# Optimization experiments

Hardware: AMD Instinct MI355X
Metric: run time of the kernel (lower is better)

Reference implementation:

```python
import jax, jax.numpy as jnp
import numpy as np

B, N, DIM = 2, 4096, 512
HEADS, HEAD_DIM = 8, 64
INNER = HEADS * HEAD_DIM


def setup_inputs() -> dict:
    key = jax.random.key(0)
    k1, k2, k3 = jax.random.split(key, 3)
    x = jax.random.normal(k1, (B, N, DIM), dtype=jnp.float32)
    w_qkv = jax.random.normal(k2, (DIM, 3 * INNER), dtype=jnp.float32) * (DIM ** -0.5)
    temperature = jnp.asarray(np.log(HEAD_DIM ** -0.5), dtype=jnp.float32)
    w_out = jax.random.normal(k3, (INNER, DIM), dtype=jnp.float32) * (INNER ** -0.5)
    b_out = jnp.zeros((DIM,), dtype=jnp.float32)
    return {"x": x, "w_qkv": w_qkv, "temperature": temperature, "w_out": w_out, "b_out": b_out}


def reference(x, w_qkv, temperature, w_out, b_out):
    b, n, _ = x.shape
    qkv = x @ w_qkv                                   # (B, N, 3*inner)
    q, k, v = jnp.split(qkv, 3, axis=-1)
    # Faithful to original: raw reshape (NOT transpose) into (B, H, N, d)
    q = q.reshape(b, HEADS, n, HEAD_DIM)
    k = k.reshape(b, HEADS, n, HEAD_DIM)
    v = v.reshape(b, HEADS, n, HEAD_DIM)
    scores = jnp.einsum('bhnd,bhmd->bhnm', q, k) * jnp.exp(temperature)
    mask = jnp.eye(n, dtype=bool)                     # diagonal self-mask
    mask_value = jnp.finfo(scores.dtype).min
    scores = jnp.where(mask, mask_value, scores)
    attn = jax.nn.softmax(scores, axis=-1)
    out = jnp.einsum('bhnm,bhmd->bhnd', attn, v)      # (B, H, N, d)
    # Faithful to original: raw reshape (NOT transpose) back to (B, N, H*d)
    out = out.reshape(b, n, HEADS * HEAD_DIM)
    return out @ w_out + b_out                        # dropout inactive at inference
```

## Files before the change

### kernel.cpp

```cpp
#include <hip/hip_runtime.h>


typedef __bf16 bf16;
typedef __bf16 bf16x8 __attribute__((ext_vector_type(8)));
typedef __bf16 bf16x4 __attribute__((ext_vector_type(4)));
typedef __bf16 bf16x2 __attribute__((ext_vector_type(2)));
typedef float  f32x4  __attribute__((ext_vector_type(4)));
typedef float  f32x16 __attribute__((ext_vector_type(16)));
typedef unsigned u32x4 __attribute__((ext_vector_type(4)));

#define MFMA_BF16(a, b, c)   __builtin_amdgcn_mfma_f32_16x16x32_bf16((a), (b), (c), 0, 0, 0)
#define MFMA32_BF16(a, b, c) __builtin_amdgcn_mfma_f32_32x32x16_bf16((a), (b), (c), 0, 0, 0)

__device__ __forceinline__ void gld_lds16(void* lds, const void* g) {
  __builtin_amdgcn_global_load_lds(
      (const __attribute__((address_space(1))) void*)g,
      (__attribute__((address_space(3))) void*)lds, 16, 0, 0);
}

__device__ __forceinline__ unsigned pkbf(float a, float b) {
  bf16x2 t; t[0] = (bf16)a; t[1] = (bf16)b;
  return __builtin_bit_cast(unsigned, t);
}


__global__ void cast4_kernel(const float* __restrict__ in, bf16* __restrict__ out, int n4) {
  int i = blockIdx.x * 256 + threadIdx.x;
  if (i >= n4) return;
  float4 v = ((const float4*)in)[i];
  bf16x4 o;
  o[0] = (bf16)v.x; o[1] = (bf16)v.y; o[2] = (bf16)v.z; o[3] = (bf16)v.w;
  *(bf16x4*)(out + 4 * i) = o;
}

__global__ void wtrans_kernel(const float* __restrict__ in, bf16* __restrict__ out, int C) {
  __shared__ float tile[64 * 65];
  const int t = threadIdx.x;
  const int c0 = blockIdx.x * 64, r0 = blockIdx.y * 64;
#pragma unroll
  for (int p = 0; p < 16; p++) {
    int idx = p * 256 + t, r = idx >> 6, c = idx & 63;
    tile[r * 65 + c] = in[(r0 + r) * C + c0 + c];
  }
  __syncthreads();
#pragma unroll
  for (int p = 0; p < 16; p++) {
    int idx = p * 256 + t, c = idx >> 6, r = idx & 63;
    out[(size_t)(c0 + c) * 512 + r0 + r] = (bf16)tile[r * 65 + c];
  }
}

__global__ void vtrans_kernel(const bf16* __restrict__ V, bf16* __restrict__ Vt) {
  __shared__ bf16 tile[64 * 65];
  const int t = threadIdx.x;
  const size_t base = (size_t)blockIdx.y << 18;
  const int n0 = blockIdx.x * 64;
#pragma unroll
  for (int p = 0; p < 16; p++) {
    int idx = p * 256 + t, r = idx >> 6, c = idx & 63;
    tile[r * 65 + c] = V[base + (size_t)(n0 + r) * 64 + c];
  }
  __syncthreads();
#pragma unroll
  for (int p = 0; p < 16; p++) {
    int idx = p * 256 + t, d = idx >> 6, n = idx & 63;
    Vt[base + (size_t)d * 4096 + n0 + n] = tile[n * 65 + d];
  }
}


template<int EPI, int WNT>
__global__ __launch_bounds__(256) void gemm_bt(
    const bf16* __restrict__ A, const bf16* __restrict__ Bt,
    bf16* __restrict__ oQ, bf16* __restrict__ oK, bf16* __restrict__ oV,
    float* __restrict__ oC, const float* __restrict__ bias,
    const float* __restrict__ temp)
{
  __shared__ bf16 As[128 * 32];
  __shared__ bf16 Bs[WNT * 32 * 32];

  const int t    = threadIdx.x;
  const int lane = t & 63;
  const int w    = t >> 6;
  const int mm   = lane & 15;
  const int q    = lane >> 4;
  const int wm   = w >> 1, wn = w & 1;
  const int m0   = blockIdx.y * 128;
  const int n0   = blockIdx.x * (WNT * 32);

  const int srow = t >> 2, sch = t & 3;
  const int gch  = sch ^ ((srow >> 1) & 3);
  const bf16* Ab = A  + (m0 + srow) * 512 + gch * 8;
  const bf16* Bb = Bt + (n0 + srow) * 512 + gch * 8;
  bf16* Asl = As + t * 8;
  bf16* Bsl = Bs + t * 8;

  const int fslot = (q ^ ((mm >> 1) & 3)) * 8;

  const f32x4 zero4 = {0.f, 0.f, 0.f, 0.f};
  f32x4 acc[4][WNT];
#pragma unroll
  for (int i = 0; i < 4; i++)
#pragma unroll
    for (int j = 0; j < WNT; j++) acc[i][j] = zero4;

  for (int k0 = 0; k0 < 512; k0 += 32) {
    __syncthreads();
    gld_lds16(Asl,        Ab + k0);
    gld_lds16(Asl + 2048, Ab + 64 * 512 + k0);
    gld_lds16(Bsl,        Bb + k0);
    if (WNT == 4) gld_lds16(Bsl + 2048, Bb + 64 * 512 + k0);
    __syncthreads();

    bf16x8 af[4], bfv[WNT];
#pragma unroll
    for (int i = 0; i < 4; i++)
      af[i] = *(const bf16x8*)(As + (wm * 64 + i * 16 + mm) * 32 + fslot);
#pragma unroll
    for (int j = 0; j < WNT; j++)
      bfv[j] = *(const bf16x8*)(Bs + (wn * (WNT * 16) + j * 16 + mm) * 32 + fslot);

#pragma unroll
    for (int i = 0; i < 4; i++)
#pragma unroll
      for (int j = 0; j < WNT; j++)
        acc[i][j] = MFMA_BF16(af[i], bfv[j], acc[i][j]);
  }

  if (EPI == 0) {
    const float scale = __expf(temp[0]) * 1.44269504088896f;
#pragma unroll
    for (int i = 0; i < 4; i++) {
      const int row = m0 + wm * 64 + i * 16 + q * 4;
#pragma unroll
      for (int j = 0; j < WNT; j++) {
        const int col = n0 + wn * (WNT * 16) + j * 16 + mm;
        bf16* dst; int c2; float s;
        if (col < 512)       { dst = oQ; c2 = col;        s = scale; }
        else if (col < 1024) { dst = oK; c2 = col - 512;  s = 1.0f;  }
        else                 { dst = oV; c2 = col - 1024; s = 1.0f;  }
#pragma unroll
        for (int r = 0; r < 4; r++)
          dst[(size_t)(row + r) * 512 + c2] = (bf16)(acc[i][j][r] * s);
      }
    }
  } else {
#pragma unroll
    for (int i = 0; i < 4; i++) {
      const int row = m0 + wm * 64 + i * 16 + q * 4;
#pragma unroll
      for (int j = 0; j < WNT; j++) {
        const int col = n0 + wn * (WNT * 16) + j * 16 + mm;
        const float b = bias[col];
#pragma unroll
        for (int r = 0; r < 4; r++)
          oC[(size_t)(row + r) * 512 + col] = acc[i][j][r] + b;
      }
    }
  }
}


__global__ __launch_bounds__(256, 2) void attn_kernel(
    const bf16* __restrict__ Q, const bf16* __restrict__ Kb,
    const bf16* __restrict__ Vt, bf16* __restrict__ O)
{
  __shared__ bf16 Ks[2][64 * 64];
  __shared__ bf16 Vs[2][64 * 64];
  __shared__ float rsum[4][32];

  const int t    = threadIdx.x;
  const int lane = t & 63;
  const int w    = t >> 6;
  const int c32  = lane & 31;
  const int h    = lane >> 5;
  const int pxa  = (lane ^ 32) << 2;
  const int bh   = blockIdx.y;
  const int q0   = blockIdx.x * 128;
  const size_t hb = (size_t)bh << 18;
  const bf16* Qh = Q  + hb;
  const bf16* Kh = Kb + hb;
  const bf16* Vh = Vt + hb;
  const int q0w  = q0 + w * 32;

  bf16x8 qf[4];
#pragma unroll
  for (int s = 0; s < 4; s++)
    qf[s] = *(const bf16x8*)(Qh + (size_t)(q0w + c32) * 64 + s * 16 + h * 8);

  f32x16 o[2];
#pragma unroll
  for (int dt = 0; dt < 2; dt++)
#pragma unroll
    for (int r = 0; r < 16; r++) o[dt][r] = 0.f;
  float lacc = 0.f;

  const int r0 = t >> 3, c0 = t & 7;
  const int g0 = c0 ^ (r0 & 7);
  const bf16* Kg = Kh + (size_t)r0 * 64 + g0 * 8;
  const bf16* Vg = Vh + (size_t)r0 * 4096 + g0 * 8;

  const int dtile  = q0w >> 6;
  const int kthalf = (q0w >> 5) & 1;

  bf16x8 pap[2][2];
  bf16x8 vfp[2][2][2];

  {
    bf16* Kn = &Ks[0][t * 8];
    bf16* Vn = &Vs[0][t * 8];
    gld_lds16(Kn,        Kg);
    gld_lds16(Kn + 2048, Kg + (size_t)32 * 64);
    gld_lds16(Vn,        Vg);
    gld_lds16(Vn + 2048, Vg + (size_t)32 * 4096);
  }

  for (int it = 0; it < 64; it++) {
    const int cur = it & 1;
    {
      const int kv = ((it + 1) & 63) * 64;
      bf16* Kn = &Ks[cur ^ 1][t * 8];
      bf16* Vn = &Vs[cur ^ 1][t * 8];
      gld_lds16(Kn,        Kg + (size_t)kv * 64);
      gld_lds16(Kn + 2048, Kg + (size_t)(kv + 32) * 64);
      gld_lds16(Vn,        Vg + kv);
      gld_lds16(Vn + 2048, Vg + (size_t)32 * 4096 + kv);
    }
    __asm__ volatile("s_waitcnt vmcnt(4)" ::: "memory");
    __builtin_amdgcn_s_barrier();
    __asm__ volatile("" ::: "memory");

    const bf16* Kc = Ks[cur];
    const bf16* Vc = Vs[cur];

    if (it) {
#pragma unroll
      for (int kt = 0; kt < 2; kt++)
#pragma unroll
        for (int s2 = 0; s2 < 2; s2++)
#pragma unroll
          for (int dt = 0; dt < 2; dt++)
            o[dt] = MFMA32_BF16(pap[kt][s2], vfp[kt][s2][dt], o[dt]);
    }

    f32x16 sv0, sv1;
#pragma unroll
    for (int r = 0; r < 16; r++) { sv0[r] = 0.f; sv1[r] = 0.f; }
    {
      bf16x8 kf[4];
#pragma unroll
      for (int s = 0; s < 4; s++)
        kf[s] = *(const bf16x8*)(Kc + c32 * 64 + (((s << 1) | h) ^ (c32 & 7)) * 8);
#pragma unroll
      for (int s = 0; s < 4; s++)
        sv0 = MFMA32_BF16(kf[s], qf[s], sv0);
    }
    {
      const int kr = 32 + c32;
      bf16x8 kf[4];
#pragma unroll
      for (int s = 0; s < 4; s++)
        kf[s] = *(const bf16x8*)(Kc + kr * 64 + (((s << 1) | h) ^ (kr & 7)) * 8);
#pragma unroll
      for (int s = 0; s < 4; s++)
        sv1 = MFMA32_BF16(kf[s], qf[s], sv1);
    }

#pragma unroll
    for (int kt = 0; kt < 2; kt++)
#pragma unroll
      for (int s2 = 0; s2 < 2; s2++)
#pragma unroll
        for (int dt = 0; dt < 2; dt++) {
          const int d = dt * 32 + c32;
          vfp[kt][s2][dt] =
              *(const bf16x8*)(Vc + d * 64 + (((((kt << 1) | s2) << 1) | h) ^ (d & 7)) * 8);
        }

    if (it == dtile) {
      if (kthalf == 0) {
#pragma unroll
        for (int r = 0; r < 16; r++)
          if (c32 == ((r & 3) + ((r >> 2) << 3) + (h << 2))) sv0[r] = -1e30f;
      } else {
#pragma unroll
        for (int r = 0; r < 16; r++)
          if (c32 == ((r & 3) + ((r >> 2) << 3) + (h << 2))) sv1[r] = -1e30f;
      }
    }

#pragma unroll
    for (int kt = 0; kt < 2; kt++) {
      float pp[16];
#pragma unroll
      for (int r = 0; r < 16; r++)
        pp[r] = __builtin_amdgcn_exp2f(kt ? sv1[r] : sv0[r]);
      float s8[8];
#pragma unroll
      for (int r = 0; r < 8; r++) s8[r] = pp[r] + pp[r + 8];
      float s4[4];
#pragma unroll
      for (int r = 0; r < 4; r++) s4[r] = s8[r] + s8[r + 4];
      lacc += (s4[0] + s4[1]) + (s4[2] + s4[3]);

#pragma unroll
      for (int s2 = 0; s2 < 2; s2++) {
        const int b = s2 * 8;
        unsigned wa = pkbf(pp[b + 0], pp[b + 1]);
        unsigned wc = pkbf(pp[b + 2], pp[b + 3]);
        unsigned wb = pkbf(pp[b + 4], pp[b + 5]);
        unsigned wd = pkbf(pp[b + 6], pp[b + 7]);
        unsigned r1 = (unsigned)__builtin_amdgcn_ds_bpermute(pxa, (int)(h ? wa : wb));
        unsigned r2 = (unsigned)__builtin_amdgcn_ds_bpermute(pxa, (int)(h ? wc : wd));
        u32x4 wv;
        wv[0] = h ? r1 : wa;
        wv[1] = h ? r2 : wc;
        wv[2] = h ? wb : r1;
        wv[3] = h ? wd : r2;
        pap[kt][s2] = __builtin_bit_cast(bf16x8, wv);
      }
    }

    __asm__ volatile("" ::: "memory");
    __builtin_amdgcn_s_barrier();
  }

#pragma unroll
  for (int kt = 0; kt < 2; kt++)
#pragma unroll
    for (int s2 = 0; s2 < 2; s2++)
#pragma unroll
      for (int dt = 0; dt < 2; dt++)
        o[dt] = MFMA32_BF16(pap[kt][s2], vfp[kt][s2][dt], o[dt]);

  const int pb = __builtin_amdgcn_ds_bpermute(pxa, __builtin_bit_cast(int, lacc));
  const float tot = lacc + __builtin_bit_cast(float, pb);

  bf16* Oh = O + hb;
  if (h == 0) rsum[w][c32] = tot;
  __asm__ volatile("s_waitcnt lgkmcnt(0)" ::: "memory");
#pragma unroll
  for (int r = 0; r < 16; r++) {
    const int row = (r & 3) + ((r >> 2) << 3) + (h << 2);
    const float rinv = 1.0f / rsum[w][row];
#pragma unroll
    for (int dt = 0; dt < 2; dt++)
      Oh[(size_t)(q0w + row) * 64 + dt * 32 + c32] = (bf16)(o[dt][r] * rinv);
  }
}


extern "C" void kernel_launch(void* const* d_in, const int* in_sizes, int n_in,
                              void* d_out, int out_size, void* d_ws, size_t ws_size,
                              hipStream_t stream) {
  const float* x      = (const float*)d_in[0];
  const float* w_qkv  = (const float*)d_in[1];
  const float* temp   = (const float*)d_in[2];
  const float* w_out  = (const float*)d_in[3];
  const float* b_out  = (const float*)d_in[4];
  float* out          = (float*)d_out;

  char* ws = (char*)d_ws;
  bf16*  Xb    = (bf16*)(ws);
  bf16*  Wt    = (bf16*)(ws + (size_t)(8u  << 20));
  bf16*  Qb    = (bf16*)(ws + (size_t)(10u << 20));
  bf16*  Kb    = (bf16*)(ws + (size_t)(18u << 20));
  bf16*  Vb    = (bf16*)(ws + (size_t)(26u << 20));
  bf16*  Vtb   = (bf16*)(ws + (size_t)(34u << 20));
  bf16*  Ob    = (bf16*)(ws + (size_t)(42u << 20));
  bf16*  Wot   = (bf16*)(ws + (size_t)(50u << 20));

  cast4_kernel<<<4096, 256, 0, stream>>>(x, Xb, (8192 * 512) / 4);
  wtrans_kernel<<<dim3(24, 8), 256, 0, stream>>>(w_qkv, Wt, 1536);
  wtrans_kernel<<<dim3(8, 8), 256, 0, stream>>>(w_out, Wot, 512);

  gemm_bt<0, 4><<<dim3(12, 64), 256, 0, stream>>>(Xb, Wt, Qb, Kb, Vb, nullptr, nullptr, temp);

  vtrans_kernel<<<dim3(64, 16), 256, 0, stream>>>(Vb, Vtb);

  attn_kernel<<<dim3(32, 16), 256, 0, stream>>>(Qb, Kb, Vtb, Ob);

  gemm_bt<1, 2><<<dim3(8, 64), 256, 0, stream>>>(Ob, Wot, nullptr, nullptr, nullptr, out, b_out, nullptr);
}
```

Measured before the change: 205.4 us.

## Double-buffer LDS tiles in bf16 GEMM to overlap global loads with MFMA

Gives the projection GEMM two LDS buffers for the A and B tiles. The next k-slice is prefetched with global_load_lds while the current slice is consumed, and manual vmcnt waits plus barriers replace the old load-then-sync pattern. The aim is to hide global memory latency behind the MFMA work. It doubles LDS use, which may reduce occupancy. It also issues a redundant wraparound load on the last iteration and depends on exact vmcnt counting being correct.

```diff
diff --git a/kernel.cpp b/kernel.cpp
--- a/kernel.cpp
+++ b/kernel.cpp
@@ -76,8 +76,8 @@
     float* __restrict__ oC, const float* __restrict__ bias,
     const float* __restrict__ temp)
 {
-  __shared__ bf16 As[128 * 32];
-  __shared__ bf16 Bs[WNT * 32 * 32];
+  __shared__ bf16 As[2][128 * 32];
+  __shared__ bf16 Bs[2][WNT * 32 * 32];
 
   const int t    = threadIdx.x;
   const int lane = t & 63;
@@ -92,8 +92,6 @@
   const int gch  = sch ^ ((srow >> 1) & 3);
   const bf16* Ab = A  + (m0 + srow) * 512 + gch * 8;
   const bf16* Bb = Bt + (n0 + srow) * 512 + gch * 8;
-  bf16* Asl = As + t * 8;
-  bf16* Bsl = Bs + t * 8;
 
   const int fslot = (q ^ ((mm >> 1) & 3)) * 8;
 
@@ -104,27 +102,46 @@
 #pragma unroll
     for (int j = 0; j < WNT; j++) acc[i][j] = zero4;
 
-  for (int k0 = 0; k0 < 512; k0 += 32) {
-    __syncthreads();
-    gld_lds16(Asl,        Ab + k0);
-    gld_lds16(Asl + 2048, Ab + 64 * 512 + k0);
-    gld_lds16(Bsl,        Bb + k0);
-    if (WNT == 4) gld_lds16(Bsl + 2048, Bb + 64 * 512 + k0);
-    __syncthreads();
+  {
+    gld_lds16(&As[0][t * 8],        Ab);
+    gld_lds16(&As[0][t * 8] + 2048, Ab + 64 * 512);
+    gld_lds16(&Bs[0][t * 8],        Bb);
+    if (WNT == 4) gld_lds16(&Bs[0][t * 8] + 2048, Bb + 64 * 512);
+  }
+
+  for (int ks = 0; ks < 16; ks++) {
+    const int cur = ks & 1;
+    {
+      const int k1 = ((ks + 1) & 15) * 32;
+      gld_lds16(&As[cur ^ 1][t * 8],        Ab + k1);
+      gld_lds16(&As[cur ^ 1][t * 8] + 2048, Ab + 64 * 512 + k1);
+      gld_lds16(&Bs[cur ^ 1][t * 8],        Bb + k1);
+      if (WNT == 4) gld_lds16(&Bs[cur ^ 1][t * 8] + 2048, Bb + 64 * 512 + k1);
+    }
+    if (WNT == 4) { __asm__ volatile("s_waitcnt vmcnt(4)" ::: "memory"); }
+    else          { __asm__ volatile("s_waitcnt vmcnt(3)" ::: "memory"); }
+    __builtin_amdgcn_s_barrier();
+    __asm__ volatile("" ::: "memory");
+
+    const bf16* Ac = As[cur];
+    const bf16* Bc = Bs[cur];
 
     bf16x8 af[4], bfv[WNT];
 #pragma unroll
     for (int i = 0; i < 4; i++)
-      af[i] = *(const bf16x8*)(As + (wm * 64 + i * 16 + mm) * 32 + fslot);
+      af[i] = *(const bf16x8*)(Ac + (wm * 64 + i * 16 + mm) * 32 + fslot);
 #pragma unroll
     for (int j = 0; j < WNT; j++)
-      bfv[j] = *(const bf16x8*)(Bs + (wn * (WNT * 16) + j * 16 + mm) * 32 + fslot);
+      bfv[j] = *(const bf16x8*)(Bc + (wn * (WNT * 16) + j * 16 + mm) * 32 + fslot);
 
 #pragma unroll
     for (int i = 0; i < 4; i++)
 #pragma unroll
       for (int j = 0; j < WNT; j++)
         acc[i][j] = MFMA_BF16(af[i], bfv[j], acc[i][j]);
+
+    __asm__ volatile("" ::: "memory");
+    __builtin_amdgcn_s_barrier();
   }
 
   if (EPI == 0) {
```

Result: no change. 206.8 us (+0.7%).
